# Kernel optimization log

Measured on AMD Instinct MI355X. Metric: run time of the kernel, lower is better.

The kernel has to match this reference:

```python
import jax, jax.numpy as jnp
import numpy as np

H = 28; W = 28; N = H * W
P = N              # padded max persistence pairs per homology dimension
T = 32             # landscape resolution
K1, K2 = 2, 3      # K_max for the two topo layers
M0_1, M0_2 = 0.05, 0.2
LIMS = ((1.0, 28.0), (1.0, 28.0))


def _make_nbrs(h, w, conn8):
    idx = np.arange(h * w).reshape(h, w)
    offs = [(-1, 0), (1, 0), (0, -1), (0, 1)]
    if conn8:
        offs += [(-1, -1), (-1, 1), (1, -1), (1, 1)]
    nbrs = []
    for i in range(h):
        for j in range(w):
            cur = [idx[i + a, j + b] for a, b in offs if 0 <= i + a < h and 0 <= j + b < w]
            nbrs.append(np.asarray(cur, np.int64))
    return nbrs

_NBR4 = _make_nbrs(H, W, False)
_NBR8 = _make_nbrs(H, W, True)


def _h0_pairs(vals, nbrs):
    # 0-dim persistence pairs of a vertex-valued sublevel filtration (union-find, elder rule)
    order = np.argsort(vals, kind="stable")
    pos = np.empty(N, np.int64); pos[order] = np.arange(N)
    parent = np.arange(N); birth = np.arange(N)
    added = np.zeros(N, bool)
    bi = np.zeros(P, np.int32); di = np.zeros(P, np.int32)
    k = 0
    def find(x):
        r = x
        while parent[r] != r: r = parent[r]
        while parent[x] != r: parent[x], x = r, parent[x]
        return r
    for v in order:
        added[v] = True
        for u in nbrs[v]:
            if not added[u]: continue
            ru, rv = find(u), find(v)
            if ru == rv: continue
            if pos[birth[ru]] <= pos[birth[rv]]:
                lb = birth[rv]; parent[rv] = ru
            else:
                lb = birth[ru]; parent[ru] = rv
            if k < P:
                bi[k] = lb; di[k] = v; k += 1
    return bi, di


def _pers_pairs_np(x):
    # x: [M, N] -> (birth_idx, death_idx) each [M, 2, P]; padded pairs point at idx 0 (zero persistence)
    x = np.asarray(x, np.float64)
    M = x.shape[0]
    bi = np.zeros((M, 2, P), np.int32); di = np.zeros((M, 2, P), np.int32)
    for m in range(M):
        b0, d0 = _h0_pairs(x[m], _NBR4)      # H0: sublevel, 4-connectivity
        b1, d1 = _h0_pairs(-x[m], _NBR8)     # H1 by Alexander duality: H0 of superlevel, 8-connectivity
        bi[m, 0], di[m, 0] = b0, d0
        bi[m, 1], di[m, 1] = d1, b1          # H1 birth = vals[d1], death = vals[b1]
    return bi, di


def _grid_d2():
    xs = np.linspace(LIMS[0][0], LIMS[0][1], H)
    ys = np.linspace(LIMS[1][0], LIMS[1][1], W)
    gx, gy = np.meshgrid(xs, ys, indexing="ij")
    pts = np.stack([gx.ravel(), gy.ravel()], 1)              # [N, 2] grid coordinates
    d2 = ((pts[:, None, :] - pts[None, :, :]) ** 2).sum(-1)  # [N, N] squared distances
    si = np.argsort(d2, axis=1, kind="stable")
    return jnp.asarray(si), jnp.asarray(np.take_along_axis(d2, si, 1), jnp.float32)

_SORT_IDX, _D2S = _grid_d2()


def dtm(x_flat, m0):
    # weighted distance-to-measure on the pixel grid, r=2; x_flat: [M, N] positive weights
    bound = m0 * jnp.sum(x_flat, -1, keepdims=True)                        # [M, 1]
    ws = x_flat[:, _SORT_IDX]                                              # [M, N, N] weights in distance order
    cum = jnp.cumsum(ws, -1)
    eff = jnp.minimum(jnp.maximum(bound[..., None] - (cum - ws), 0.0), ws) # effective mass per neighbor
    return jnp.sqrt(jnp.sum(eff * _D2S, -1) / bound)                       # [M, N]


def _landscape(vals, bi, di, start, end, K):
    # persistence landscape lambda_k sampled on T points from (birth, death) critical-vertex indices
    M = vals.shape[0]
    mi = jnp.arange(M)[:, None, None]
    b = vals[mi, bi]; d = vals[mi, di]                                     # [M, 2, P]
    t = jnp.linspace(start, end, T, dtype=vals.dtype)                      # [T]
    tent = jnp.maximum(jnp.minimum(t - b[..., None], d[..., None] - t), 0.0)  # [M, 2, P, T]
    lam, _ = jax.lax.top_k(jnp.swapaxes(tent, -1, -2), K)                  # [M, 2, T, K]
    return jnp.swapaxes(lam, -1, -2).reshape(M, 2 * K * T)                 # [M, dims*K*T]


def pl_features(vals, start, end, K):
    M = vals.shape[0]
    bi, di = jax.pure_callback(
        _pers_pairs_np,
        (jax.ShapeDtypeStruct((M, 2, P), np.int32),
         jax.ShapeDtypeStruct((M, 2, P), np.int32)),
        jax.lax.stop_gradient(vals))
    return _landscape(vals, bi, di, start, end, K)


def setup_inputs():
    key = jax.random.key(0)
    ks = jax.random.split(key, 7)
    B = 64
    return {
        "input": jax.random.uniform(ks[0], (B, 1, H, W), jnp.float32, 1e-3, 1.0),
        "w_g1": 0.1 * jax.random.normal(ks[1], (32, 2 * K1 * T), jnp.float32),
        "b_g1": 0.1 * jax.random.normal(ks[2], (32,), jnp.float32),
        "w_g2": 0.1 * jax.random.normal(ks[3], (32, 2 * K2 * T), jnp.float32),
        "b_g2": 0.1 * jax.random.normal(ks[4], (32,), jnp.float32),
        "w_fc": 0.1 * jax.random.normal(ks[5], (10, 64), jnp.float32),
        "b_fc": 0.1 * jax.random.normal(ks[6], (10,), jnp.float32),
    }


def reference(input, w_g1, b_g1, w_g2, b_g2, w_fc, b_fc):
    x_flat = input.reshape(-1, N)                                        # num_channels = 1
    f1 = dtm(x_flat, M0_1)
    f2 = dtm(x_flat, M0_2)
    x1 = jax.nn.relu(pl_features(f1, 0.0, 7.0, K1) @ w_g1.T + b_g1)      # topo layer 1 (start=0, end=7, K=2)
    x2 = jax.nn.relu(pl_features(f2, 1.0, 8.0, K2) @ w_g2.T + b_g2)      # topo layer 2 (start=1, end=8, K=3)
    return jnp.concatenate([x1, x2], -1) @ w_fc.T + b_fc                 # [B, num_classes]
```

## Files before the change

### kernel.cpp

```cpp
#include <hip/hip_runtime.h>

#define HW 28
#define NPIX 784
#define NIMG 64
#define MAXD2 1459
#define MAXREC 5504

#define DXPK 41048u
#define DYPK 34949u

__global__ void consts_sums_kernel(unsigned int* __restrict__ TPK,
                                   const float* __restrict__ x,
                                   float* __restrict__ sums,
                                   float* __restrict__ xT) {
    int tid = threadIdx.x;
    if (blockIdx.x >= NPIX) {
        int m = blockIdx.x - NPIX;
        const float* xr = x + m * NPIX;
        float acc = 0.f;
        for (int j = tid; j < NPIX; j += 256) {
            float v = xr[j];
            xT[j * NIMG + m] = v;
            acc += v;
        }
        for (int off = 32; off > 0; off >>= 1) acc += __shfl_down(acc, off, 64);
        __shared__ float red[4];
        int lane = tid & 63, w = tid >> 6;
        if (lane == 0) red[w] = acc;
        __syncthreads();
        if (tid == 0) sums[m] = red[0] + red[1] + red[2] + red[3];
        return;
    }
    __shared__ int cnt[MAXD2];
    __shared__ int d2v[NPIX];
    __shared__ int wtot[4];
    int i = blockIdx.x;
    for (int b = tid; b < MAXD2; b += 256) cnt[b] = 0;
    __syncthreads();
    int ii = i / HW, ij = i % HW;
    for (int j = tid; j < NPIX; j += 256) {
        int di = ii - j / HW, dj = ij - j % HW;
        int d = di * di + dj * dj;
        d2v[j] = d;
        atomicAdd(&cnt[d], 1);
    }
    __syncthreads();
    int b0 = tid * 6;
    int lc[6];
    int s0 = 0;
    #pragma unroll
    for (int t = 0; t < 6; ++t) {
        int b = b0 + t;
        lc[t] = (b < MAXD2) ? cnt[b] : 0;
        s0 += lc[t];
    }
    int lane = tid & 63, wv = tid >> 6;
    int v = s0;
    for (int off = 1; off < 64; off <<= 1) {
        int t2 = __shfl_up(v, off, 64);
        if (lane >= off) v += t2;
    }
    if (lane == 63) wtot[wv] = v;
    __syncthreads();
    int wadd = 0;
    for (int w2 = 0; w2 < wv; ++w2) wadd += wtot[w2];
    int run = wadd + v - s0;
    __syncthreads();
    #pragma unroll
    for (int t = 0; t < 6; ++t) {
        int b = b0 + t;
        if (b < MAXD2) { cnt[b] = run; run += lc[t]; }
    }
    __syncthreads();
    for (int j = tid; j < NPIX; j += 256) {
        int d = d2v[j];
        int slot = atomicAdd(&cnt[d], 1);
        TPK[i * NPIX + slot] = (unsigned)j | ((unsigned)d << 16);
    }
}

__global__ void __launch_bounds__(64) dtm_kernel(const unsigned int* __restrict__ TPK,
                                                 const float* __restrict__ xT,
                                                 const float* __restrict__ sums,
                                                 float* __restrict__ F) {
    int lane = threadIdx.x;
    int i = blockIdx.x;
    float s = sums[lane];
    float bound1 = 0.05f * s, bound2 = 0.2f * s;
    const unsigned int* tp = TPK + (size_t)i * NPIX;
    float cum = 0.f, acc1 = 0.f, acc2 = 0.f;
    for (int t0 = 0; t0 < NPIX; t0 += 8) {
        unsigned int e[8];
        #pragma unroll
        for (int u = 0; u < 8; ++u) e[u] = tp[t0 + u];
        float w[8];
        #pragma unroll
        for (int u = 0; u < 8; ++u) w[u] = xT[(e[u] & 0xffffu) * NIMG + lane];
        #pragma unroll
        for (int u = 0; u < 8; ++u) {
            float d2 = (float)(e[u] >> 16);
            float ce = cum;
            cum += w[u];
            acc1 += fminf(fmaxf(bound1 - ce, 0.f), w[u]) * d2;
            acc2 += fminf(fmaxf(bound2 - ce, 0.f), w[u]) * d2;
        }
        if (__ballot(cum < bound2) == 0ull) break;
    }
    F[0 * NIMG * NPIX + lane * NPIX + i] = sqrtf(acc1 / bound1);
    F[1 * NIMG * NPIX + lane * NPIX + i] = sqrtf(acc2 / bound2);
}

template<int NN>
__device__ int uf_basin_run(const int* posA, const int* ordA,
                            int* bas, unsigned int* pb, int* comp,
                            int* recs, int* pairsI,
                            int2* mergeLDS, int* shInts, int* wtot8) {
    const int tid = threadIdx.x;
    const int lane = tid & 63, wv = tid >> 6;

    for (int s = tid; s < NPIX; s += 512) {
        int si = s / HW, sj = s % HW;
        int bestPos = posA[s], best = s;
        #pragma unroll
        for (int o = 0; o < NN; ++o) {
            int dx = ((DXPK >> (2 * o)) & 3) - 1;
            int dy = ((DYPK >> (2 * o)) & 3) - 1;
            int ui = si + dx, uj = sj + dy;
            if ((unsigned)ui < (unsigned)HW && (unsigned)uj < (unsigned)HW) {
                int u = ui * HW + uj;
                int pu = posA[u];
                if (pu < bestPos) { bestPos = pu; best = u; }
            }
        }
        bas[s] = best;
    }
    __syncthreads();

    for (int it = 0; it < 10; ++it) {
        int changed = 0;
        for (int s = tid; s < NPIX; s += 512) {
            int b = bas[s];
            int bb = bas[b];
            if (bb != b) { bas[s] = bb; changed = 1; }
        }
        if (__syncthreads_count(changed) == 0) break;
    }

    for (int s = tid; s < NPIX; s += 512)
        pb[s] = ((unsigned)posA[s] << 10) | (unsigned)bas[s];
    __syncthreads();

    int nrec = 0;
    for (int c = 0; c < 2; ++c) {
        int r = c * 512 + tid;
        int cnt = 0;
        int myr[NN - 1];
        int got[NN - 1];
        #pragma unroll
        for (int t = 0; t < NN - 1; ++t) { got[t] = -1; myr[t] = 0; }
        if (r > 0 && r < NPIX) {
            int v = ordA[r];
            int vi = v / HW, vj = v % HW;
            int pivot = (int)(pb[v] & 1023u);
            #pragma unroll
            for (int o = 0; o < NN; ++o) {
                int dx = ((DXPK >> (2 * o)) & 3) - 1;
                int dy = ((DYPK >> (2 * o)) & 3) - 1;
                int ui = vi + dx, uj = vj + dy;
                if ((unsigned)ui < (unsigned)HW && (unsigned)uj < (unsigned)HW) {
                    int u = ui * HW + uj;
                    unsigned e = pb[u];
                    if ((int)(e >> 10) < r) {
                        int b = (int)(e & 1023u);
                        bool dup = (b == pivot);
                        #pragma unroll
                        for (int t = 0; t < NN - 1; ++t) dup = dup || (got[t] == b);
                        if (!dup) {
                            #pragma unroll
                            for (int t = 0; t < NN - 1; ++t)
                                if (t == cnt) { got[t] = b; myr[t] = (v << 20) | (pivot << 10) | b; }
                            cnt++;
                        }
                    }
                }
            }
        }
        int p = cnt;
        for (int off = 1; off < 64; off <<= 1) {
            int t2 = __shfl_up(p, off, 64);
            if (lane >= off) p += t2;
        }
        if (lane == 63) wtot8[wv] = p;
        __syncthreads();
        int wadd = 0;
        for (int w2 = 0; w2 < wv; ++w2) wadd += wtot8[w2];
        int tot = 0;
        #pragma unroll
        for (int w2 = 0; w2 < 8; ++w2) tot += wtot8[w2];
        int excl = wadd + p - cnt;
        #pragma unroll
        for (int t = 0; t < NN - 1; ++t)
            if (t < cnt) recs[nrec + excl + t] = myr[t];
        nrec += tot;
        __syncthreads();
    }

    int k = 0;
    for (int base = 0; base < nrec; base += 64) {
        int nrem = 0;
        if (wv == 0) {
            int idx = base + lane;
            int rec = (idx < nrec) ? recs[idx] : 0;
            int pa = (rec >> 10) & 1023, pbn = rec & 1023;
            int ka = 0, kb = 0;
            if (idx < nrec) { ka = comp[pa]; kb = comp[pbn]; }
            for (;;) {
                unsigned long long d = __ballot(ka != kb);
                if (d == 0ull) break;
                int i = (int)__ffsll((long long)d) - 1;
                int sA = __builtin_amdgcn_readlane(ka, i);
                int sB = __builtin_amdgcn_readlane(kb, i);
                int w = min(sA, sB), l = max(sA, sB);
                int sv = __builtin_amdgcn_readlane(rec, i) >> 20;
                if (lane == 0) {
                    pairsI[k] = (l & 1023) | (sv << 10);
                    mergeLDS[nrem] = make_int2(l, w);
                }
                k++;
                ka = (ka == l) ? w : ka;
                kb = (kb == l) ? w : kb;
                nrem++;
                if (nrem == 63) {
                    for (int s = lane; s < NPIX; s += 64) {
                        int cv = comp[s], c0 = cv;
                        for (int e = 0; e < nrem; ++e) {
                            int2 me = mergeLDS[e];
                            cv = (cv == me.x) ? me.y : cv;
                        }
                        if (cv != c0) comp[s] = cv;
                    }
                    if (idx < nrec) { ka = comp[pa]; kb = comp[pbn]; }
                    nrem = 0;
                }
            }
            if (lane == 0) shInts[0] = nrem;
        }
        __syncthreads();
        int nr = shInts[0];
        if (nr > 0) {
            for (int s = tid; s < NPIX; s += 512) {
                int cv = comp[s], c0 = cv;
                for (int e = 0; e < nr; ++e) {
                    int2 me = mergeLDS[e];
                    cv = (cv == me.x) ? me.y : cv;
                }
                if (cv != c0) comp[s] = cv;
            }
        }
        __syncthreads();
    }
    if (tid == 0) shInts[1] = k;
    __syncthreads();
    return shInts[1];
}

__global__ void __launch_bounds__(512) uf_land_kernel(const float* __restrict__ F,
                                                      float* __restrict__ LAM1,
                                                      float* __restrict__ LAM2) {
    __shared__ int posA[NPIX], ordA[NPIX], bas[NPIX], comp[NPIX], pairsI[NPIX];
    __shared__ unsigned int ukey[NPIX];
    __shared__ float fv[NPIX];
    __shared__ float2 pairs[NPIX];
    __shared__ int recs[MAXREC];
    __shared__ int2 mergeLDS[64];
    __shared__ int shInts[2];
    __shared__ int wtot8[8];
    int tid = threadIdx.x;
    int task = blockIdx.x;
    int feat = task >> 7;
    int dir = (task >> 6) & 1;
    int m = task & 63;
    const float* fr = F + feat * NIMG * NPIX + m * NPIX;

    for (int j = tid; j < NPIX; j += 512) {
        float f = fr[j];
        fv[j] = f;
        unsigned int b = __float_as_uint(f);
        ukey[j] = dir ? ~b : b;
    }
    __syncthreads();

    {
        unsigned long long pki[2];
        int rank[2] = {0, 0};
        bool val[2];
        #pragma unroll
        for (int r = 0; r < 2; ++r) {
            int i = tid + 512 * r;
            val[r] = (i < NPIX);
            pki[r] = val[r] ? (((unsigned long long)ukey[i] << 10) | (unsigned)i) : 0ull;
        }
        const uint4* k4 = (const uint4*)ukey;
        for (int c = 0; c < NPIX / 4; ++c) {
            uint4 kv = k4[c];
            unsigned q = 4u * c;
            unsigned long long p0 = ((unsigned long long)kv.x << 10) | q;
            unsigned long long p1 = ((unsigned long long)kv.y << 10) | (q + 1);
            unsigned long long p2 = ((unsigned long long)kv.z << 10) | (q + 2);
            unsigned long long p3 = ((unsigned long long)kv.w << 10) | (q + 3);
            #pragma unroll
            for (int r = 0; r < 2; ++r) {
                rank[r] += (int)(p0 < pki[r]) + (int)(p1 < pki[r])
                         + (int)(p2 < pki[r]) + (int)(p3 < pki[r]);
            }
        }
        #pragma unroll
        for (int r = 0; r < 2; ++r) {
            if (val[r]) {
                int i = tid + 512 * r;
                posA[i] = rank[r];
                ordA[rank[r]] = i;
            }
        }
    }
    __syncthreads();
    for (int s = tid; s < NPIX; s += 512) comp[s] = (posA[s] << 10) | s;

    int k;
    if (dir == 0) k = uf_basin_run<4>(posA, ordA, bas, ukey, comp, recs, pairsI,
                                      mergeLDS, shInts, wtot8);
    else          k = uf_basin_run<8>(posA, ordA, bas, ukey, comp, recs, pairsI,
                                      mergeLDS, shInts, wtot8);

    for (int s = tid; s < k; s += 512) {
        int p = pairsI[s];
        float fb = fv[p & 1023], fd = fv[p >> 10];
        pairs[s] = dir ? make_float2(fd, fb) : make_float2(fb, fd);
    }
    __syncthreads();

    if (tid < 32) {
        int t = tid;
        float start = (feat == 0) ? 0.f : 1.f;
        float end   = (feat == 0) ? 7.f : 8.f;
        float tv = start + (end - start) * ((float)t / 31.f);
        float v0 = 0.f, v1 = 0.f, v2 = 0.f;
        for (int p = 0; p < k; ++p) {
            float2 bd = pairs[p];
            float tent = fmaxf(fminf(tv - bd.x, bd.y - tv), 0.f);
            if (tent > v0)      { v2 = v1; v1 = v0; v0 = tent; }
            else if (tent > v1) { v2 = v1; v1 = tent; }
            else if (tent > v2) { v2 = tent; }
        }
        if (feat == 0) {
            float* lam = LAM1 + m * 128 + dir * 64;
            lam[0 * 32 + t] = v0;
            lam[1 * 32 + t] = v1;
        } else {
            float* lam = LAM2 + m * 192 + dir * 96;
            lam[0 * 32 + t] = v0;
            lam[1 * 32 + t] = v1;
            lam[2 * 32 + t] = v2;
        }
    }
}

__global__ void mlp_kernel(const float* __restrict__ LAM1, const float* __restrict__ LAM2,
                           const float* __restrict__ w1, const float* __restrict__ b1,
                           const float* __restrict__ w2, const float* __restrict__ b2,
                           const float* __restrict__ wf, const float* __restrict__ bf,
                           float* __restrict__ out) {
    __shared__ float xc[64];
    int m = blockIdx.x;
    int n = threadIdx.x;
    if (n < 32) {
        float acc = b1[n];
        const float* l = LAM1 + m * 128;
        for (int c = 0; c < 128; ++c) acc += w1[n * 128 + c] * l[c];
        xc[n] = fmaxf(acc, 0.f);
    } else {
        int n2 = n - 32;
        float acc = b2[n2];
        const float* l = LAM2 + m * 192;
        for (int c = 0; c < 192; ++c) acc += w2[n2 * 192 + c] * l[c];
        xc[n] = fmaxf(acc, 0.f);
    }
    __syncthreads();
    if (n < 10) {
        float acc = bf[n];
        for (int c = 0; c < 64; ++c) acc += wf[n * 64 + c] * xc[c];
        out[m * 10 + n] = acc;
    }
}

extern "C" void kernel_launch(void* const* d_in, const int* in_sizes, int n_in,
                              void* d_out, int out_size, void* d_ws, size_t ws_size,
                              hipStream_t stream) {
    const float* x  = (const float*)d_in[0];
    const float* w1 = (const float*)d_in[1];
    const float* b1 = (const float*)d_in[2];
    const float* w2 = (const float*)d_in[3];
    const float* b2 = (const float*)d_in[4];
    const float* wf = (const float*)d_in[5];
    const float* bf = (const float*)d_in[6];
    float* out = (float*)d_out;

    char* ws = (char*)d_ws;
    size_t off = 0;
    unsigned int* TPK = (unsigned int*)(ws + off); off += (size_t)NPIX * NPIX * 4;
    float* XT   = (float*)(ws + off); off += (size_t)NPIX * NIMG * 4;
    float* SUMS = (float*)(ws + off); off += 256;
    float* F    = (float*)(ws + off); off += (size_t)2 * NIMG * NPIX * 4;
    float* LAM1 = (float*)(ws + off); off += (size_t)NIMG * 128 * 4;
    float* LAM2 = (float*)(ws + off); off += (size_t)NIMG * 192 * 4;

    consts_sums_kernel<<<NPIX + NIMG, 256, 0, stream>>>(TPK, x, SUMS, XT);
    dtm_kernel<<<NPIX, 64, 0, stream>>>(TPK, XT, SUMS, F);
    uf_land_kernel<<<256, 512, 0, stream>>>(F, LAM1, LAM2);
    mlp_kernel<<<NIMG, 64, 0, stream>>>(LAM1, LAM2, w1, b1, w2, b2, wf, bf, out);
}
```

Measured before the change: 138.8 us.

## Fuse distance-sort into DTM kernel via LDS and widen union-find blocks to 1024

New measurement: 135.7 us. 2.3% less time.

```diff
diff --git a/kernel.cpp b/kernel.cpp
--- a/kernel.cpp
+++ b/kernel.cpp
@@ -9,90 +9,81 @@
 #define DXPK 41048u
 #define DYPK 34949u
 
-__global__ void consts_sums_kernel(unsigned int* __restrict__ TPK,
-                                   const float* __restrict__ x,
-                                   float* __restrict__ sums,
-                                   float* __restrict__ xT) {
+__global__ void sums_transpose_kernel(const float* __restrict__ x,
+                                      float* __restrict__ sums,
+                                      float* __restrict__ xT) {
     int tid = threadIdx.x;
-    if (blockIdx.x >= NPIX) {
-        int m = blockIdx.x - NPIX;
-        const float* xr = x + m * NPIX;
-        float acc = 0.f;
-        for (int j = tid; j < NPIX; j += 256) {
-            float v = xr[j];
-            xT[j * NIMG + m] = v;
-            acc += v;
-        }
-        for (int off = 32; off > 0; off >>= 1) acc += __shfl_down(acc, off, 64);
-        __shared__ float red[4];
-        int lane = tid & 63, w = tid >> 6;
-        if (lane == 0) red[w] = acc;
-        __syncthreads();
-        if (tid == 0) sums[m] = red[0] + red[1] + red[2] + red[3];
-        return;
-    }
+    int m = blockIdx.x;
+    const float* xr = x + m * NPIX;
+    float acc = 0.f;
+    for (int j = tid; j < NPIX; j += 256) {
+        float v = xr[j];
+        xT[j * NIMG + m] = v;
+        acc += v;
+    }
+    for (int off = 32; off > 0; off >>= 1) acc += __shfl_down(acc, off, 64);
+    __shared__ float red[4];
+    int lane = tid & 63, w = tid >> 6;
+    if (lane == 0) red[w] = acc;
+    __syncthreads();
+    if (tid == 0) sums[m] = red[0] + red[1] + red[2] + red[3];
+}
+
+__global__ void __launch_bounds__(64) dtm_kernel(const float* __restrict__ xT,
+                                                 const float* __restrict__ sums,
+                                                 float* __restrict__ F) {
     __shared__ int cnt[MAXD2];
-    __shared__ int d2v[NPIX];
-    __shared__ int wtot[4];
+    __shared__ unsigned int tpk[NPIX];
+    int lane = threadIdx.x;
     int i = blockIdx.x;
-    for (int b = tid; b < MAXD2; b += 256) cnt[b] = 0;
-    __syncthreads();
     int ii = i / HW, ij = i % HW;
-    for (int j = tid; j < NPIX; j += 256) {
-        int di = ii - j / HW, dj = ij - j % HW;
-        int d = di * di + dj * dj;
-        d2v[j] = d;
-        atomicAdd(&cnt[d], 1);
-    }
-    __syncthreads();
-    int b0 = tid * 6;
-    int lc[6];
-    int s0 = 0;
+
+    for (int b = lane; b < MAXD2; b += 64) cnt[b] = 0;
+    int dloc[13], jloc[13];
     #pragma unroll
-    for (int t = 0; t < 6; ++t) {
+    for (int u = 0; u < 13; ++u) {
+        int j = u * 64 + lane;
+        int d = 0;
+        if (j < NPIX) {
+            int di = ii - j / HW, dj = ij - j % HW;
+            d = di * di + dj * dj;
+            atomicAdd(&cnt[d], 1);
+        }
+        dloc[u] = d; jloc[u] = j;
+    }
+    int b0 = lane * 23;
+    int lsum = 0;
+    #pragma unroll
+    for (int t = 0; t < 23; ++t) {
         int b = b0 + t;
-        lc[t] = (b < MAXD2) ? cnt[b] : 0;
-        s0 += lc[t];
-    }
-    int lane = tid & 63, wv = tid >> 6;
-    int v = s0;
+        if (b < MAXD2) lsum += cnt[b];
+    }
+    int v = lsum;
     for (int off = 1; off < 64; off <<= 1) {
         int t2 = __shfl_up(v, off, 64);
         if (lane >= off) v += t2;
     }
-    if (lane == 63) wtot[wv] = v;
-    __syncthreads();
-    int wadd = 0;
-    for (int w2 = 0; w2 < wv; ++w2) wadd += wtot[w2];
-    int run = wadd + v - s0;
-    __syncthreads();
+    int run = v - lsum;
     #pragma unroll
-    for (int t = 0; t < 6; ++t) {
+    for (int t = 0; t < 23; ++t) {
         int b = b0 + t;
-        if (b < MAXD2) { cnt[b] = run; run += lc[t]; }
-    }
-    __syncthreads();
-    for (int j = tid; j < NPIX; j += 256) {
-        int d = d2v[j];
-        int slot = atomicAdd(&cnt[d], 1);
-        TPK[i * NPIX + slot] = (unsigned)j | ((unsigned)d << 16);
-    }
-}
-
-__global__ void __launch_bounds__(64) dtm_kernel(const unsigned int* __restrict__ TPK,
-                                                 const float* __restrict__ xT,
-                                                 const float* __restrict__ sums,
-                                                 float* __restrict__ F) {
-    int lane = threadIdx.x;
-    int i = blockIdx.x;
+        if (b < MAXD2) { int c = cnt[b]; cnt[b] = run; run += c; }
+    }
+    #pragma unroll
+    for (int u = 0; u < 13; ++u) {
+        if (jloc[u] < NPIX) {
+            int slot = atomicAdd(&cnt[dloc[u]], 1);
+            tpk[slot] = (unsigned)jloc[u] | ((unsigned)dloc[u] << 16);
+        }
+    }
+
     float s = sums[lane];
     float bound1 = 0.05f * s, bound2 = 0.2f * s;
-    const unsigned int* tp = TPK + (size_t)i * NPIX;
     float cum = 0.f, acc1 = 0.f, acc2 = 0.f;
     for (int t0 = 0; t0 < NPIX; t0 += 8) {
         unsigned int e[8];
         #pragma unroll
-        for (int u = 0; u < 8; ++u) e[u] = tp[t0 + u];
+        for (int u = 0; u < 8; ++u) e[u] = tpk[t0 + u];
         float w[8];
         #pragma unroll
         for (int u = 0; u < 8; ++u) w[u] = xT[(e[u] & 0xffffu) * NIMG + lane];
@@ -114,11 +105,11 @@
 __device__ int uf_basin_run(const int* posA, const int* ordA,
                             int* bas, unsigned int* pb, int* comp,
                             int* recs, int* pairsI,
-                            int2* mergeLDS, int* shInts, int* wtot8) {
+                            int2* mergeLDS, int* shInts, int* wtot16) {
     const int tid = threadIdx.x;
     const int lane = tid & 63, wv = tid >> 6;
 
-    for (int s = tid; s < NPIX; s += 512) {
+    for (int s = tid; s < NPIX; s += 1024) {
         int si = s / HW, sj = s % HW;
         int bestPos = posA[s], best = s;
         #pragma unroll
@@ -138,7 +129,7 @@
 
     for (int it = 0; it < 10; ++it) {
         int changed = 0;
-        for (int s = tid; s < NPIX; s += 512) {
+        for (int s = tid; s < NPIX; s += 1024) {
             int b = bas[s];
             int bb = bas[b];
             if (bb != b) { bas[s] = bb; changed = 1; }
@@ -146,13 +137,13 @@
         if (__syncthreads_count(changed) == 0) break;
     }
 
-    for (int s = tid; s < NPIX; s += 512)
+    for (int s = tid; s < NPIX; s += 1024)
         pb[s] = ((unsigned)posA[s] << 10) | (unsigned)bas[s];
     __syncthreads();
 
     int nrec = 0;
-    for (int c = 0; c < 2; ++c) {
-        int r = c * 512 + tid;
+    {
+        int r = tid;
         int cnt = 0;
         int myr[NN - 1];
         int got[NN - 1];
@@ -190,18 +181,18 @@
             int t2 = __shfl_up(p, off, 64);
             if (lane >= off) p += t2;
         }
-        if (lane == 63) wtot8[wv] = p;
+        if (lane == 63) wtot16[wv] = p;
         __syncthreads();
         int wadd = 0;
-        for (int w2 = 0; w2 < wv; ++w2) wadd += wtot8[w2];
+        for (int w2 = 0; w2 < wv; ++w2) wadd += wtot16[w2];
         int tot = 0;
         #pragma unroll
-        for (int w2 = 0; w2 < 8; ++w2) tot += wtot8[w2];
+        for (int w2 = 0; w2 < 16; ++w2) tot += wtot16[w2];
         int excl = wadd + p - cnt;
         #pragma unroll
         for (int t = 0; t < NN - 1; ++t)
-            if (t < cnt) recs[nrec + excl + t] = myr[t];
-        nrec += tot;
+            if (t < cnt) recs[excl + t] = myr[t];
+        nrec = tot;
         __syncthreads();
     }
 
@@ -248,7 +239,7 @@
         __syncthreads();
         int nr = shInts[0];
         if (nr > 0) {
-            for (int s = tid; s < NPIX; s += 512) {
+            for (int s = tid; s < NPIX; s += 1024) {
                 int cv = comp[s], c0 = cv;
                 for (int e = 0; e < nr; ++e) {
                     int2 me = mergeLDS[e];
@@ -264,9 +255,9 @@
     return shInts[1];
 }
 
-__global__ void __launch_bounds__(512) uf_land_kernel(const float* __restrict__ F,
-                                                      float* __restrict__ LAM1,
-                                                      float* __restrict__ LAM2) {
+__global__ void __launch_bounds__(1024) uf_land_kernel(const float* __restrict__ F,
+                                                       float* __restrict__ LAM1,
+                                                       float* __restrict__ LAM2) {
     __shared__ int posA[NPIX], ordA[NPIX], bas[NPIX], comp[NPIX], pairsI[NPIX];
     __shared__ unsigned int ukey[NPIX];
     __shared__ float fv[NPIX];
@@ -274,7 +265,7 @@
     __shared__ int recs[MAXREC];
     __shared__ int2 mergeLDS[64];
     __shared__ int shInts[2];
-    __shared__ int wtot8[8];
+    __shared__ int wtot16[16];
     int tid = threadIdx.x;
     int task = blockIdx.x;
     int feat = task >> 7;
@@ -282,7 +273,7 @@
     int m = task & 63;
     const float* fr = F + feat * NIMG * NPIX + m * NPIX;
 
-    for (int j = tid; j < NPIX; j += 512) {
+    for (int j = tid; j < NPIX; j += 1024) {
         float f = fr[j];
         fv[j] = f;
         unsigned int b = __float_as_uint(f);
@@ -291,15 +282,10 @@
     __syncthreads();
 
     {
-        unsigned long long pki[2];
-        int rank[2] = {0, 0};
-        bool val[2];
-        #pragma unroll
-        for (int r = 0; r < 2; ++r) {
-            int i = tid + 512 * r;
-            val[r] = (i < NPIX);
-            pki[r] = val[r] ? (((unsigned long long)ukey[i] << 10) | (unsigned)i) : 0ull;
-        }
+        bool val = (tid < NPIX);
+        unsigned long long pki = val
+            ? (((unsigned long long)ukey[tid] << 10) | (unsigned)tid) : 0ull;
+        int rank = 0;
         const uint4* k4 = (const uint4*)ukey;
         for (int c = 0; c < NPIX / 4; ++c) {
             uint4 kv = k4[c];
@@ -308,31 +294,24 @@
             unsigned long long p1 = ((unsigned long long)kv.y << 10) | (q + 1);
             unsigned long long p2 = ((unsigned long long)kv.z << 10) | (q + 2);
             unsigned long long p3 = ((unsigned long long)kv.w << 10) | (q + 3);
-            #pragma unroll
-            for (int r = 0; r < 2; ++r) {
-                rank[r] += (int)(p0 < pki[r]) + (int)(p1 < pki[r])
-                         + (int)(p2 < pki[r]) + (int)(p3 < pki[r]);
-            }
-        }
-        #pragma unroll
-        for (int r = 0; r < 2; ++r) {
-            if (val[r]) {
-                int i = tid + 512 * r;
-                posA[i] = rank[r];
-                ordA[rank[r]] = i;
-            }
-        }
-    }
-    __syncthreads();
-    for (int s = tid; s < NPIX; s += 512) comp[s] = (posA[s] << 10) | s;
+            rank += (int)(p0 < pki) + (int)(p1 < pki)
+                  + (int)(p2 < pki) + (int)(p3 < pki);
+        }
+        if (val) {
+            posA[tid] = rank;
+            ordA[rank] = tid;
+        }
+    }
+    __syncthreads();
+    for (int s = tid; s < NPIX; s += 1024) comp[s] = (posA[s] << 10) | s;
 
     int k;
     if (dir == 0) k = uf_basin_run<4>(posA, ordA, bas, ukey, comp, recs, pairsI,
-                                      mergeLDS, shInts, wtot8);
+                                      mergeLDS, shInts, wtot16);
     else          k = uf_basin_run<8>(posA, ordA, bas, ukey, comp, recs, pairsI,
-                                      mergeLDS, shInts, wtot8);
-
-    for (int s = tid; s < k; s += 512) {
+                                      mergeLDS, shInts, wtot16);
+
+    for (int s = tid; s < k; s += 1024) {
         int p = pairsI[s];
         float fb = fv[p & 1023], fd = fv[p >> 10];
         pairs[s] = dir ? make_float2(fd, fb) : make_float2(fb, fd);
@@ -407,15 +386,14 @@
 
     char* ws = (char*)d_ws;
     size_t off = 0;
-    unsigned int* TPK = (unsigned int*)(ws + off); off += (size_t)NPIX * NPIX * 4;
     float* XT   = (float*)(ws + off); off += (size_t)NPIX * NIMG * 4;
     float* SUMS = (float*)(ws + off); off += 256;
     float* F    = (float*)(ws + off); off += (size_t)2 * NIMG * NPIX * 4;
     float* LAM1 = (float*)(ws + off); off += (size_t)NIMG * 128 * 4;
     float* LAM2 = (float*)(ws + off); off += (size_t)NIMG * 192 * 4;
 
-    consts_sums_kernel<<<NPIX + NIMG, 256, 0, stream>>>(TPK, x, SUMS, XT);
-    dtm_kernel<<<NPIX, 64, 0, stream>>>(TPK, XT, SUMS, F);
-    uf_land_kernel<<<256, 512, 0, stream>>>(F, LAM1, LAM2);
+    sums_transpose_kernel<<<NIMG, 256, 0, stream>>>(x, SUMS, XT);
+    dtm_kernel<<<NPIX, 64, 0, stream>>>(XT, SUMS, F);
+    uf_land_kernel<<<256, 1024, 0, stream>>>(F, LAM1, LAM2);
     mlp_kernel<<<NIMG, 64, 0, stream>>>(LAM1, LAM2, w1, b1, w2, b2, wf, bf, out);
 }
```

## Run union-find landscape kernel with 1024 threads and precomputed 64-bit sort keys

Applied to the files above, without the earlier changes.

Result: faster. 122.6 us, median of 2 (-11.7%).

```diff
diff --git a/kernel.cpp b/kernel.cpp
--- a/kernel.cpp
+++ b/kernel.cpp
@@ -114,11 +114,11 @@
 __device__ int uf_basin_run(const int* posA, const int* ordA,
                             int* bas, unsigned int* pb, int* comp,
                             int* recs, int* pairsI,
-                            int2* mergeLDS, int* shInts, int* wtot8) {
+                            int2* mergeLDS, int* shInts, int* wtot16) {
     const int tid = threadIdx.x;
     const int lane = tid & 63, wv = tid >> 6;
 
-    for (int s = tid; s < NPIX; s += 512) {
+    for (int s = tid; s < NPIX; s += 1024) {
         int si = s / HW, sj = s % HW;
         int bestPos = posA[s], best = s;
         #pragma unroll
@@ -138,7 +138,7 @@
 
     for (int it = 0; it < 10; ++it) {
         int changed = 0;
-        for (int s = tid; s < NPIX; s += 512) {
+        for (int s = tid; s < NPIX; s += 1024) {
             int b = bas[s];
             int bb = bas[b];
             if (bb != b) { bas[s] = bb; changed = 1; }
@@ -146,13 +146,13 @@
         if (__syncthreads_count(changed) == 0) break;
     }
 
-    for (int s = tid; s < NPIX; s += 512)
+    for (int s = tid; s < NPIX; s += 1024)
         pb[s] = ((unsigned)posA[s] << 10) | (unsigned)bas[s];
     __syncthreads();
 
     int nrec = 0;
-    for (int c = 0; c < 2; ++c) {
-        int r = c * 512 + tid;
+    {
+        int r = tid;
         int cnt = 0;
         int myr[NN - 1];
         int got[NN - 1];
@@ -190,18 +190,18 @@
             int t2 = __shfl_up(p, off, 64);
             if (lane >= off) p += t2;
         }
-        if (lane == 63) wtot8[wv] = p;
+        if (lane == 63) wtot16[wv] = p;
         __syncthreads();
         int wadd = 0;
-        for (int w2 = 0; w2 < wv; ++w2) wadd += wtot8[w2];
+        for (int w2 = 0; w2 < wv; ++w2) wadd += wtot16[w2];
         int tot = 0;
         #pragma unroll
-        for (int w2 = 0; w2 < 8; ++w2) tot += wtot8[w2];
+        for (int w2 = 0; w2 < 16; ++w2) tot += wtot16[w2];
         int excl = wadd + p - cnt;
         #pragma unroll
         for (int t = 0; t < NN - 1; ++t)
-            if (t < cnt) recs[nrec + excl + t] = myr[t];
-        nrec += tot;
+            if (t < cnt) recs[excl + t] = myr[t];
+        nrec = tot;
         __syncthreads();
     }
 
@@ -248,7 +248,7 @@
         __syncthreads();
         int nr = shInts[0];
         if (nr > 0) {
-            for (int s = tid; s < NPIX; s += 512) {
+            for (int s = tid; s < NPIX; s += 1024) {
                 int cv = comp[s], c0 = cv;
                 for (int e = 0; e < nr; ++e) {
                     int2 me = mergeLDS[e];
@@ -264,17 +264,17 @@
     return shInts[1];
 }
 
-__global__ void __launch_bounds__(512) uf_land_kernel(const float* __restrict__ F,
-                                                      float* __restrict__ LAM1,
-                                                      float* __restrict__ LAM2) {
+__global__ void __launch_bounds__(1024) uf_land_kernel(const float* __restrict__ F,
+                                                       float* __restrict__ LAM1,
+                                                       float* __restrict__ LAM2) {
     __shared__ int posA[NPIX], ordA[NPIX], bas[NPIX], comp[NPIX], pairsI[NPIX];
-    __shared__ unsigned int ukey[NPIX];
+    __shared__ unsigned int pbArr[NPIX];
+    __shared__ alignas(16) unsigned long long key64[NPIX];
     __shared__ float fv[NPIX];
-    __shared__ float2 pairs[NPIX];
     __shared__ int recs[MAXREC];
     __shared__ int2 mergeLDS[64];
     __shared__ int shInts[2];
-    __shared__ int wtot8[8];
+    __shared__ int wtot16[16];
     int tid = threadIdx.x;
     int task = blockIdx.x;
     int feat = task >> 7;
@@ -282,62 +282,34 @@
     int m = task & 63;
     const float* fr = F + feat * NIMG * NPIX + m * NPIX;
 
-    for (int j = tid; j < NPIX; j += 512) {
+    for (int j = tid; j < NPIX; j += 1024) {
         float f = fr[j];
         fv[j] = f;
         unsigned int b = __float_as_uint(f);
-        ukey[j] = dir ? ~b : b;
-    }
-    __syncthreads();
-
-    {
-        unsigned long long pki[2];
-        int rank[2] = {0, 0};
-        bool val[2];
-        #pragma unroll
-        for (int r = 0; r < 2; ++r) {
-            int i = tid + 512 * r;
-            val[r] = (i < NPIX);
-            pki[r] = val[r] ? (((unsigned long long)ukey[i] << 10) | (unsigned)i) : 0ull;
-        }
-        const uint4* k4 = (const uint4*)ukey;
-        for (int c = 0; c < NPIX / 4; ++c) {
-            uint4 kv = k4[c];
-            unsigned q = 4u * c;
-            unsigned long long p0 = ((unsigned long long)kv.x << 10) | q;
-            unsigned long long p1 = ((unsigned long long)kv.y << 10) | (q + 1);
-            unsigned long long p2 = ((unsigned long long)kv.z << 10) | (q + 2);
-            unsigned long long p3 = ((unsigned long long)kv.w << 10) | (q + 3);
-            #pragma unroll
-            for (int r = 0; r < 2; ++r) {
-                rank[r] += (int)(p0 < pki[r]) + (int)(p1 < pki[r])
-                         + (int)(p2 < pki[r]) + (int)(p3 < pki[r]);
-            }
-        }
-        #pragma unroll
-        for (int r = 0; r < 2; ++r) {
-            if (val[r]) {
-                int i = tid + 512 * r;
-                posA[i] = rank[r];
-                ordA[rank[r]] = i;
-            }
-        }
-    }
-    __syncthreads();
-    for (int s = tid; s < NPIX; s += 512) comp[s] = (posA[s] << 10) | s;
+        if (dir) b = ~b;
+        key64[j] = ((unsigned long long)b << 10) | (unsigned)j;
+    }
+    __syncthreads();
+
+    if (tid < NPIX) {
+        unsigned long long pki = key64[tid];
+        int rank = 0;
+        const ulonglong2* k2 = (const ulonglong2*)key64;
+        for (int c = 0; c < NPIX / 2; ++c) {
+            ulonglong2 kv = k2[c];
+            rank += (int)(kv.x < pki) + (int)(kv.y < pki);
+        }
+        posA[tid] = rank;
+        ordA[rank] = tid;
+    }
+    __syncthreads();
+    for (int s = tid; s < NPIX; s += 1024) comp[s] = (posA[s] << 10) | s;
 
     int k;
-    if (dir == 0) k = uf_basin_run<4>(posA, ordA, bas, ukey, comp, recs, pairsI,
-                                      mergeLDS, shInts, wtot8);
-    else          k = uf_basin_run<8>(posA, ordA, bas, ukey, comp, recs, pairsI,
-                                      mergeLDS, shInts, wtot8);
-
-    for (int s = tid; s < k; s += 512) {
-        int p = pairsI[s];
-        float fb = fv[p & 1023], fd = fv[p >> 10];
-        pairs[s] = dir ? make_float2(fd, fb) : make_float2(fb, fd);
-    }
-    __syncthreads();
+    if (dir == 0) k = uf_basin_run<4>(posA, ordA, bas, pbArr, comp, recs, pairsI,
+                                      mergeLDS, shInts, wtot16);
+    else          k = uf_basin_run<8>(posA, ordA, bas, pbArr, comp, recs, pairsI,
+                                      mergeLDS, shInts, wtot16);
 
     if (tid < 32) {
         int t = tid;
@@ -346,8 +318,11 @@
         float tv = start + (end - start) * ((float)t / 31.f);
         float v0 = 0.f, v1 = 0.f, v2 = 0.f;
         for (int p = 0; p < k; ++p) {
-            float2 bd = pairs[p];
-            float tent = fmaxf(fminf(tv - bd.x, bd.y - tv), 0.f);
+            int pi = pairsI[p];
+            float fb = fv[pi & 1023], fd = fv[pi >> 10];
+            float bb = dir ? fd : fb;
+            float dd = dir ? fb : fd;
+            float tent = fmaxf(fminf(tv - bb, dd - tv), 0.f);
             if (tent > v0)      { v2 = v1; v1 = v0; v0 = tent; }
             else if (tent > v1) { v2 = v1; v1 = tent; }
             else if (tent > v2) { v2 = tent; }
@@ -416,6 +391,6 @@
 
     consts_sums_kernel<<<NPIX + NIMG, 256, 0, stream>>>(TPK, x, SUMS, XT);
     dtm_kernel<<<NPIX, 64, 0, stream>>>(TPK, XT, SUMS, F);
-    uf_land_kernel<<<256, 512, 0, stream>>>(F, LAM1, LAM2);
+    uf_land_kernel<<<256, 1024, 0, stream>>>(F, LAM1, LAM2);
     mlp_kernel<<<NIMG, 64, 0, stream>>>(LAM1, LAM2, w1, b1, w2, b2, wf, bf, out);
 }
```
